# Performance work log

Hardware: AMD Instinct MI355X
Metric: run time of the kernel (lower is better)

Reference implementation:

```python
import jax, jax.numpy as jnp
import numpy as np


def _gcn(h, W, b, src, dst):
    # PyG GCNConv: x @ W, then symmetric-normalized aggregation over edges
    # (edge list already includes self-loops), bias added after.
    n = h.shape[0]
    deg = jnp.zeros((n,), h.dtype).at[dst].add(jnp.ones((), h.dtype))
    dinv = jnp.where(deg > 0, jax.lax.rsqrt(deg), jnp.zeros((), h.dtype))
    norm = dinv[src] * dinv[dst]  # [E]
    m = h @ W                     # [N, d_h]
    out = jnp.zeros_like(m).at[dst].add(norm[:, None] * m[src])
    return out + b


def setup_inputs() -> dict:
    key = jax.random.key(0)
    F, K = 1000, 100              # files, blocks per file
    N = F * K                     # total blocks
    D_SEM, D_STR = 768, 256
    D_H, D_SH, D_PR, NPROJ = 512, 256, 256, 100

    # sliding-window (window=2) edges within each file, bidirectional, + self loops
    base = np.arange(N)
    pos = base % K
    s_l, d_l = [], []
    for d in (1, 2):
        i = base[pos < K - d]
        j = i + d
        s_l += [i, j]
        d_l += [j, i]
    s_l.append(base)  # self loops (GCNConv add_self_loops)
    d_l.append(base)
    src = jnp.asarray(np.concatenate(s_l), dtype=jnp.int32)
    dst = jnp.asarray(np.concatenate(d_l), dtype=jnp.int32)
    seg_ids = jnp.asarray(base // K, dtype=jnp.int32)  # file id per block (CSR blk_ptr equivalent)

    ks = jax.random.split(key, 16)
    def w(k, shape):
        return jax.random.normal(k, shape, jnp.float32) * 0.02
    z = lambda n: jnp.zeros((n,), jnp.float32)

    return dict(
        h_sem=jax.random.normal(ks[0], (N, D_SEM), jnp.float32),
        e_struct=jax.random.normal(ks[1], (N, D_STR), jnp.float32),
        W_fusion=w(ks[2], (D_SEM + D_STR, D_H)), b_fusion=z(D_H),
        W_g1=w(ks[3], (D_H, D_H)), b_g1=z(D_H),
        W_g2=w(ks[4], (D_H, D_H)), b_g2=z(D_H),
        W_att=w(ks[5], (D_H, D_H)), b_att=z(D_H),
        context=w(ks[6], (D_H,)),
        W_sh1=w(ks[7], (D_H, D_SH)), b_sh1=z(D_SH),
        W_sh2=w(ks[8], (D_SH, D_SH)), b_sh2=z(D_SH),
        W_pr1=w(ks[9], (D_H, D_PR)), b_pr1=z(D_PR),
        W_pr2=w(ks[10], (D_PR, D_PR)), b_pr2=z(D_PR),
        W_dpr=w(ks[11], (D_PR, NPROJ)), b_dpr=z(NPROJ),
        W_bug=w(ks[12], (D_H, 1)), b_bug=z(1),
        src=src, dst=dst, seg_ids=seg_ids, num_files=F,
    )


def reference(h_sem, e_struct, W_fusion, b_fusion, W_g1, b_g1, W_g2, b_g2,
              W_att, b_att, context, W_sh1, b_sh1, W_sh2, b_sh2,
              W_pr1, b_pr1, W_pr2, b_pr2, W_dpr, b_dpr, W_bug, b_bug,
              src, dst, seg_ids, num_files):
    # fusion of semantic + structural features
    h0 = jnp.concatenate([h_sem, e_struct], axis=1) @ W_fusion + b_fusion  # [N, d_h]
    h1 = jax.nn.relu(_gcn(h0, W_g1, b_g1, src, dst))
    h_blk = _gcn(h1, W_g2, b_g2, src, dst)                                # [N, d_h]

    # ragged attention pooling over per-file segments (vectorized segment softmax)
    scores = jnp.tanh(h_blk @ W_att + b_att) @ context                    # [N]
    seg_max = jax.ops.segment_max(scores, seg_ids, num_segments=num_files)
    ex = jnp.exp(scores - seg_max[seg_ids])
    seg_sum = jax.ops.segment_sum(ex, seg_ids, num_segments=num_files)
    alpha = ex / seg_sum[seg_ids]                                         # [N]
    h_file = jax.ops.segment_sum(alpha[:, None] * h_blk, seg_ids,
                                 num_segments=num_files)                  # [F, d_h]

    z_sh = jax.nn.relu(h_file @ W_sh1 + b_sh1) @ W_sh2 + b_sh2            # [F, d_sh]
    z_pr = jax.nn.relu(h_file @ W_pr1 + b_pr1) @ W_pr2 + b_pr2            # [F, d_pr]
    logits_pr_dom = z_pr @ W_dpr + b_dpr                                  # [F, num_projects]
    logit_bug = h_file @ W_bug + b_bug                                    # [F, 1]
    loss_ortho = jnp.mean((z_sh.T @ z_pr) ** 2)                           # disentanglement penalty
    return (h_blk, alpha, h_file, z_sh, z_pr, logits_pr_dom, logit_bug, loss_ortho)
```

## Files before the change

### kernel.cpp

```cpp
#include <hip/hip_runtime.h>

typedef unsigned short u16;
typedef unsigned int   u32;
typedef __attribute__((ext_vector_type(8))) short  short8;
typedef __attribute__((ext_vector_type(4))) float  floatx4;

#define DEV __device__ __forceinline__

DEV float bf2f(u16 u){ return __uint_as_float(((u32)u) << 16); }
DEV u16 f2bf(float x){
  u32 u = __float_as_uint(x);
  u += 0x7FFFu + ((u >> 16) & 1u);
  return (u16)(u >> 16);
}
DEV float blo(u32 u){ return __uint_as_float(u << 16); }
DEV float bhi(u32 u){ return __uint_as_float(u & 0xffff0000u); }

DEV void async16(const void* g, void* l){
  __builtin_amdgcn_global_load_lds((__attribute__((address_space(1))) void*)g,
                                   (__attribute__((address_space(3))) void*)l,
                                   16, 0, 0);
}

constexpr int NN   = 100000;
constexpr int FF   = 1000;
constexpr int KPF  = 100;
constexpr int DH   = 512;

constexpr size_t OUT_HBLK  = 0;
constexpr size_t OUT_ALPHA = 51200000;
constexpr size_t OUT_HFILE = 51300000;
constexpr size_t OUT_ZSH   = 51812000;
constexpr size_t OUT_ZPR   = 52068000;
constexpr size_t OUT_LOG   = 52324000;
constexpr size_t OUT_BUG   = 52424000;
constexpr size_t OUT_LOSS  = 52425000;

constexpr size_t WS_A      = 0;
constexpr size_t WS_M1     = 0;
constexpr size_t WS_H1     = 102400000;
constexpr size_t WS_HBLK   = 0;
constexpr size_t WS_H0     = 204800000;
constexpr size_t WS_M2     = 204800000;
constexpr size_t WS_SCOREP = 307200000;
constexpr size_t WS_WT     = 308800000;
constexpr size_t WS_HFILEB = 312300000;
constexpr size_t WS_TSH    = 313400000;
constexpr size_t WS_TPR    = 314000000;
constexpr size_t WS_ZPRB   = 314600000;
constexpr size_t WS_ORTHOP = 315200000;

constexpr int WT_FUS = 0;
constexpr int WT_G1  = 524288;
constexpr int WT_G2  = 786432;
constexpr int WT_ATT = 1048576;
constexpr int WT_SH1 = 1310720;
constexpr int WT_SH2 = 1441792;
constexpr int WT_PR1 = 1507328;
constexpr int WT_PR2 = 1638400;
constexpr int WT_DPR = 1703936;
constexpr int WT_TOT = 1729536;

struct PrepTab {
  const float* src[9];
  int K[9];
  int N[9];
  int prefix[10];
};

__global__ __launch_bounds__(256) void prep_w(PrepTab t, u16* __restrict__ dst){
  int gid = blockIdx.x * 256 + threadIdx.x;
  if (gid >= t.prefix[9]) return;
  int i = 0;
  while (gid >= t.prefix[i+1]) ++i;
  int e  = gid - t.prefix[i];
  int Ni = t.N[i];
  int k  = e / Ni;
  int n  = e - k * Ni;
  dst[t.prefix[i] + (size_t)n * t.K[i] + k] = f2bf(t.src[i][(size_t)k * Ni + n]);
}

__global__ __launch_bounds__(256) void build_A(const float* __restrict__ hsem,
                                               const float* __restrict__ est,
                                               u16* __restrict__ out){
  int gid = blockIdx.x * 256 + threadIdx.x;
  int row = gid >> 7;
  int c   = (gid & 127) << 3;
  const float* src = (c < 768) ? (hsem + (size_t)row * 768 + c)
                               : (est  + (size_t)row * 256 + (c - 768));
  float4 v0 = *(const float4*)src;
  float4 v1 = *(const float4*)(src + 4);
  uint4 o;
  o.x = (u32)f2bf(v0.x) | ((u32)f2bf(v0.y) << 16);
  o.y = (u32)f2bf(v0.z) | ((u32)f2bf(v0.w) << 16);
  o.z = (u32)f2bf(v1.x) | ((u32)f2bf(v1.y) << 16);
  o.w = (u32)f2bf(v1.z) | ((u32)f2bf(v1.w) << 16);
  *(uint4*)(out + (size_t)row * 1024 + c) = o;
}

template<int MODE, bool BIAS>
__global__ __launch_bounds__(512, 2) void gemm256(
    const u16* __restrict__ A, const u16* __restrict__ B,
    int M, int N, int K,
    const float* __restrict__ bias,
    u16* __restrict__ outb,
    const float* __restrict__ ctx, float* __restrict__ scorep)
{
  extern __shared__ u16 S[];
  const int tid  = threadIdx.x;
  const int wid  = tid >> 6, lane = tid & 63;
  const int lq   = lane >> 4, lr = lane & 15;

  const int ny  = N >> 8;
  const int nwg = (int)gridDim.x;
  const int q   = nwg >> 3, r = nwg & 7;
  const int xcd = (int)blockIdx.x & 7, pos = (int)blockIdx.x >> 3;
  const int lid = (xcd < r ? xcd * (q + 1) : r * (q + 1) + (xcd - r) * q) + pos;
  const int ty  = lid % ny, tx = lid / ny;
  const int m0  = tx << 8, n0 = ty << 8;

  const int wr = wid >> 2, wc = wid & 3;
  const int wrow = wr << 7, wcol = wc << 6;

  const int srow = (wid << 3) + (lane >> 3);
  const int scol = ((lane & 7) ^ (lane >> 3)) << 3;
  const u16* pa[4];
  const u16* pb[4];
  #pragma unroll
  for (int h = 0; h < 2; ++h)
    #pragma unroll
    for (int j = 0; j < 2; ++j) {
      int ra = m0 + h * 128 + j * 64 + srow;  ra = min(ra, M - 1);
      int rb = n0 + h * 128 + j * 64 + srow;
      pa[h * 2 + j] = A + (size_t)ra * K + scol;
      pb[h * 2 + j] = B + (size_t)rb * K + scol;
    }

  auto STAGE = [&](int p){
    char* base = (char*)S + (p << 16) + (wid << 10);
    #pragma unroll
    for (int h = 0; h < 2; ++h)
      #pragma unroll
      for (int j = 0; j < 2; ++j) {
        async16(pa[h * 2 + j], base + h * 16384 + j * 8192);
        async16(pb[h * 2 + j], base + 32768 + h * 16384 + j * 8192);
        pa[h * 2 + j] += 64;  pb[h * 2 + j] += 64;
      }
  };

  floatx4 acc[8][4];
  #pragma unroll
  for (int i = 0; i < 8; ++i)
    #pragma unroll
    for (int j = 0; j < 4; ++j)
      acc[i][j] = floatx4{0.f, 0.f, 0.f, 0.f};

  const int NT = K >> 6;
  STAGE(0);
  STAGE(1);

  const int rsl = lr & 7;
  for (int kt = 0; kt < NT; ++kt) {
    if (kt + 1 < NT) asm volatile("s_waitcnt vmcnt(8)" ::: "memory");
    else             asm volatile("s_waitcnt vmcnt(0)" ::: "memory");
    __builtin_amdgcn_s_barrier();
    __builtin_amdgcn_sched_barrier(0);
    const u16* ap = S + ((kt & 1) << 15);
    const u16* bp = ap + 16384;
    #pragma unroll
    for (int k2 = 0; k2 < 2; ++k2) {
      short8 af[8], bf[4];
      const int sl = ((k2 << 2) | lq) ^ rsl;
      #pragma unroll
      for (int mi = 0; mi < 8; ++mi)
        af[mi] = *(const short8*)(ap + ((wrow + mi * 16 + lr) << 6) + (sl << 3));
      #pragma unroll
      for (int ni = 0; ni < 4; ++ni)
        bf[ni] = *(const short8*)(bp + ((wcol + ni * 16 + lr) << 6) + (sl << 3));
      __builtin_amdgcn_s_setprio(1);
      #pragma unroll
      for (int mi = 0; mi < 8; ++mi)
        #pragma unroll
        for (int ni = 0; ni < 4; ++ni)
          acc[mi][ni] = __builtin_amdgcn_mfma_f32_16x16x32_bf16(af[mi], bf[ni], acc[mi][ni], 0, 0, 0);
      __builtin_amdgcn_s_setprio(0);
    }
    __builtin_amdgcn_s_barrier();
    __builtin_amdgcn_sched_barrier(0);
    if (kt + 2 < NT) STAGE(kt & 1);
  }

  if constexpr (MODE == 3) {
    #pragma unroll
    for (int mi = 0; mi < 8; ++mi) {
      #pragma unroll
      for (int r2 = 0; r2 < 4; ++r2) {
        float psum = 0.f;
        #pragma unroll
        for (int ni = 0; ni < 4; ++ni) {
          int gc = n0 + wcol + ni * 16 + lr;
          psum += tanhf(acc[mi][ni][r2] + bias[gc]) * ctx[gc];
        }
        psum += __shfl_xor(psum, 1); psum += __shfl_xor(psum, 2);
        psum += __shfl_xor(psum, 4); psum += __shfl_xor(psum, 8);
        int gr = m0 + wrow + mi * 16 + (lq << 2) + r2;
        if (lr == 0 && gr < M) scorep[(size_t)ty * M + gr] = psum;
      }
    }
  } else {
    #pragma unroll
    for (int mi = 0; mi < 8; ++mi) {
      int grb = m0 + wrow + mi * 16 + (lq << 2);
      #pragma unroll
      for (int ni = 0; ni < 4; ++ni) {
        int gc = n0 + wcol + ni * 16 + lr;
        float bv = BIAS ? bias[gc] : 0.f;
        #pragma unroll
        for (int r2 = 0; r2 < 4; ++r2) {
          int gr = grb + r2;
          if (gr < M) outb[(size_t)gr * N + gc] = f2bf(acc[mi][ni][r2] + bv);
        }
      }
    }
  }
}

template<int MODE, bool BIAS, bool RELU>
__global__ __launch_bounds__(256) void gemm_bt(
    const u16* __restrict__ A, const u16* __restrict__ B,
    int M, int N, int K, int ny,
    const float* __restrict__ bias,
    u16* __restrict__ outb, float* __restrict__ outf,
    int ldc, int nvalid,
    const float* __restrict__ ctx, float* __restrict__ scorep)
{
  __shared__ u16 As[3 * 4096];
  __shared__ u16 Bs[3 * 4096];
  const int tid  = threadIdx.x;
  const int wave = tid >> 6, lane = tid & 63;

  const int nwg = (int)gridDim.x;
  const int q   = nwg >> 3, r = nwg & 7;
  const int xcd = (int)blockIdx.x & 7, pos = (int)blockIdx.x >> 3;
  const int lid = (xcd < r ? xcd * (q + 1) : r * (q + 1) + (xcd - r) * q) + pos;
  const int ty  = lid % ny, tx = lid / ny;
  const int m0  = tx << 7, n0 = ty << 7;

  const int wm = (wave & 1) << 6, wn = (wave >> 1) << 6;
  const int lq = lane >> 4, lr = lane & 15;

  floatx4 acc[4][4];
  #pragma unroll
  for (int i = 0; i < 4; ++i)
    #pragma unroll
    for (int j = 0; j < 4; ++j)
      acc[i][j] = floatx4{0.f, 0.f, 0.f, 0.f};

  int arow = m0 + (wave << 4) + (lane >> 2);
  int ar0 = min(arow, M - 1);
  int ar1 = min(arow + 64, M - 1);
  int brow = n0 + (wave << 4) + (lane >> 2);
  int br0 = min(brow, N - 1);
  int br1 = min(brow + 64, N - 1);
  const int kc = (((lane & 3) ^ ((lane >> 3) & 3)) << 3);
  const u16* ga0 = A + (size_t)ar0 * K + kc;
  const u16* ga1 = A + (size_t)ar1 * K + kc;
  const u16* gb0 = B + (size_t)br0 * K + kc;
  const u16* gb1 = B + (size_t)br1 * K + kc;

  auto STAGE = [&](int buf){
    u16* as = As + (buf << 12);
    u16* bs = Bs + (buf << 12);
    async16(ga0, as + (wave << 9));
    async16(ga1, as + 2048 + (wave << 9));
    async16(gb0, bs + (wave << 9));
    async16(gb1, bs + 2048 + (wave << 9));
    ga0 += 32; ga1 += 32; gb0 += 32; gb1 += 32;
  };

  const int nIt = K >> 5;
  STAGE(0);
  if (nIt > 1) STAGE(1);
  const int rsw = (lr >> 1) & 3;
  int bt = 0;
  for (int it = 0; it < nIt; ++it) {
    if (it + 1 < nIt) asm volatile("s_waitcnt vmcnt(4) lgkmcnt(0)" ::: "memory");
    else              asm volatile("s_waitcnt vmcnt(0) lgkmcnt(0)" ::: "memory");
    __builtin_amdgcn_s_barrier();
    __builtin_amdgcn_sched_barrier(0);
    if (it + 2 < nIt) { int b2 = bt + 2; if (b2 >= 3) b2 -= 3; STAGE(b2); }
    const u16* as = As + (bt << 12);
    const u16* bs = Bs + (bt << 12);
    short8 af[4], bfr[4];
    #pragma unroll
    for (int mi = 0; mi < 4; ++mi)
      af[mi] = *(const short8*)(as + ((wm + mi * 16 + lr) << 5) + ((lq ^ rsw) << 3));
    #pragma unroll
    for (int ni = 0; ni < 4; ++ni)
      bfr[ni] = *(const short8*)(bs + ((wn + ni * 16 + lr) << 5) + ((lq ^ rsw) << 3));
    #pragma unroll
    for (int mi = 0; mi < 4; ++mi)
      #pragma unroll
      for (int ni = 0; ni < 4; ++ni)
        acc[mi][ni] = __builtin_amdgcn_mfma_f32_16x16x32_bf16(af[mi], bfr[ni], acc[mi][ni], 0, 0, 0);
    if (++bt == 3) bt = 0;
  }

  if constexpr (MODE == 3) {
    #pragma unroll
    for (int mi = 0; mi < 4; ++mi) {
      #pragma unroll
      for (int r2 = 0; r2 < 4; ++r2) {
        float p = 0.f;
        #pragma unroll
        for (int ni = 0; ni < 4; ++ni) {
          int gc = n0 + wn + ni * 16 + lr;
          p += tanhf(acc[mi][ni][r2] + bias[gc]) * ctx[gc];
        }
        p += __shfl_xor(p, 1); p += __shfl_xor(p, 2);
        p += __shfl_xor(p, 4); p += __shfl_xor(p, 8);
        int gr = m0 + wm + mi * 16 + lq * 4 + r2;
        if (lr == 0 && gr < M) scorep[(size_t)ty * M + gr] = p;
      }
    }
  } else {
    #pragma unroll
    for (int mi = 0; mi < 4; ++mi) {
      int grb = m0 + wm + mi * 16 + lq * 4;
      #pragma unroll
      for (int ni = 0; ni < 4; ++ni) {
        int gc = n0 + wn + ni * 16 + lr;
        if (gc >= nvalid) continue;
        float bv = BIAS ? bias[gc] : 0.f;
        #pragma unroll
        for (int r2 = 0; r2 < 4; ++r2) {
          int gr = grb + r2;
          if (gr >= M) continue;
          float v = acc[mi][ni][r2] + bv;
          if (RELU) v = fmaxf(v, 0.f);
          if (MODE == 0 || MODE == 2) outb[(size_t)gr * ldc + gc] = f2bf(v);
          if (MODE == 1 || MODE == 2) outf[(size_t)gr * ldc + gc] = v;
        }
      }
    }
  }
}

DEV float dinv_of(int p){
  return rsqrtf((float)(1 + min(p, 2) + min(99 - p, 2)));
}

template<bool RELU, bool DUAL>
__global__ __launch_bounds__(256) void agg_k(const u16* __restrict__ m,
                                             const float* __restrict__ bias,
                                             u16* __restrict__ outb,
                                             float* __restrict__ outf){
  int gid = blockIdx.x * 256 + threadIdx.x;
  int row = gid >> 6;
  int c   = (gid & 63) << 3;
  int pos = row % KPF;
  float ds = dinv_of(pos);
  float a0=0,a1=0,a2=0,a3=0,a4=0,a5=0,a6=0,a7=0;
  #pragma unroll
  for (int d = -2; d <= 2; ++d) {
    int p2 = pos + d;
    if (p2 < 0 || p2 >= KPF) continue;
    float w = ds * dinv_of(p2);
    uint4 v = *(const uint4*)(m + (size_t)(row + d) * DH + c);
    a0 += w * blo(v.x); a1 += w * bhi(v.x);
    a2 += w * blo(v.y); a3 += w * bhi(v.y);
    a4 += w * blo(v.z); a5 += w * bhi(v.z);
    a6 += w * blo(v.w); a7 += w * bhi(v.w);
  }
  float o[8] = {a0,a1,a2,a3,a4,a5,a6,a7};
  #pragma unroll
  for (int j = 0; j < 8; ++j) {
    o[j] += bias[c + j];
    if (RELU) o[j] = fmaxf(o[j], 0.f);
  }
  uint4 st;
  st.x = (u32)f2bf(o[0]) | ((u32)f2bf(o[1]) << 16);
  st.y = (u32)f2bf(o[2]) | ((u32)f2bf(o[3]) << 16);
  st.z = (u32)f2bf(o[4]) | ((u32)f2bf(o[5]) << 16);
  st.w = (u32)f2bf(o[6]) | ((u32)f2bf(o[7]) << 16);
  *(uint4*)(outb + (size_t)row * DH + c) = st;
  if (DUAL) {
    float4 f0 = {o[0], o[1], o[2], o[3]};
    float4 f1 = {o[4], o[5], o[6], o[7]};
    *(float4*)(outf + (size_t)row * DH + c)     = f0;
    *(float4*)(outf + (size_t)row * DH + c + 4) = f1;
  }
}

__global__ __launch_bounds__(256) void pool_k(const float* __restrict__ sp,
                                              const u16* __restrict__ hblk,
                                              float* __restrict__ alpha_out,
                                              float* __restrict__ hfile_f,
                                              u16* __restrict__ hfile_b){
  int f = blockIdx.x, tid = threadIdx.x;
  __shared__ float sAl[KPF];
  __shared__ float red[8];
  float s = -INFINITY;
  if (tid < KPF) {
    int r = f * KPF + tid;
    s = sp[r] + sp[NN + r];
  }
  float mx = s;
  for (int off = 32; off >= 1; off >>= 1) mx = fmaxf(mx, __shfl_xor(mx, off));
  if ((tid & 63) == 0) red[tid >> 6] = mx;
  __syncthreads();
  mx = fmaxf(fmaxf(red[0], red[1]), fmaxf(red[2], red[3]));
  float ex = (tid < KPF) ? expf(s - mx) : 0.f;
  float sm = ex;
  for (int off = 32; off >= 1; off >>= 1) sm += __shfl_xor(sm, off);
  if ((tid & 63) == 0) red[4 + (tid >> 6)] = sm;
  __syncthreads();
  sm = red[4] + red[5] + red[6] + red[7];
  float al = ex / sm;
  if (tid < KPF) { alpha_out[(size_t)f * KPF + tid] = al; sAl[tid] = al; }
  __syncthreads();
  const u16* base = hblk + (size_t)f * KPF * DH;
  float acc0 = 0.f, acc1 = 0.f;
  for (int i = 0; i < KPF; ++i) {
    float w = sAl[i];
    acc0 += w * bf2f(base[i * DH + tid]);
    acc1 += w * bf2f(base[i * DH + 256 + tid]);
  }
  hfile_f[(size_t)f * DH + tid]       = acc0;
  hfile_f[(size_t)f * DH + 256 + tid] = acc1;
  hfile_b[(size_t)f * DH + tid]       = f2bf(acc0);
  hfile_b[(size_t)f * DH + 256 + tid] = f2bf(acc1);
}

__global__ __launch_bounds__(256) void bug_k(const float* __restrict__ hfile,
                                             const float* __restrict__ w,
                                             const float* __restrict__ b,
                                             float* __restrict__ out){
  int row  = blockIdx.x * 4 + (threadIdx.x >> 6);
  int lane = threadIdx.x & 63;
  const float* h = hfile + (size_t)row * DH;
  float s = 0.f;
  #pragma unroll
  for (int j = 0; j < 8; ++j) s += h[lane + j * 64] * w[lane + j * 64];
  for (int off = 32; off >= 1; off >>= 1) s += __shfl_xor(s, off);
  if (lane == 0) out[row] = s + b[0];
}

__global__ __launch_bounds__(256) void ortho_k(const float* __restrict__ zsh,
                                               const float* __restrict__ zpr,
                                               float* __restrict__ part){
  int bi = blockIdx.x >> 4, bj = blockIdx.x & 15;
  int ty = threadIdx.x >> 4, tx = threadIdx.x & 15;
  __shared__ float sa[64 * 16], sb[64 * 16];
  float acc = 0.f;
  for (int k0 = 0; k0 < FF; k0 += 64) {
    #pragma unroll
    for (int q = 0; q < 4; ++q) {
      int kk = ty + q * 16;
      int k  = k0 + kk;
      float va = 0.f, vb = 0.f;
      if (k < FF) {
        va = zsh[(size_t)k * 256 + bi * 16 + tx];
        vb = zpr[(size_t)k * 256 + bj * 16 + tx];
      }
      sa[kk * 16 + tx] = va;
      sb[kk * 16 + tx] = vb;
    }
    __syncthreads();
    #pragma unroll 8
    for (int kk = 0; kk < 64; ++kk) acc += sa[kk * 16 + ty] * sb[kk * 16 + tx];
    __syncthreads();
  }
  float ssq = acc * acc;
  for (int off = 32; off >= 1; off >>= 1) ssq += __shfl_xor(ssq, off);
  __shared__ float r[4];
  if ((threadIdx.x & 63) == 0) r[threadIdx.x >> 6] = ssq;
  __syncthreads();
  if (threadIdx.x == 0) part[blockIdx.x] = r[0] + r[1] + r[2] + r[3];
}

__global__ __launch_bounds__(256) void ortho_fin(const float* __restrict__ part,
                                                 float* __restrict__ out){
  int tid = threadIdx.x;
  float s = part[tid];
  for (int off = 32; off >= 1; off >>= 1) s += __shfl_xor(s, off);
  __shared__ float r[4];
  if ((tid & 63) == 0) r[tid >> 6] = s;
  __syncthreads();
  if (tid == 0) out[0] = (r[0] + r[1] + r[2] + r[3]) * (1.0f / 65536.0f);
}

extern "C" void kernel_launch(void* const* d_in, const int* in_sizes, int n_in,
                              void* d_out, int out_size, void* d_ws, size_t ws_size,
                              hipStream_t stream) {
  const float* h_sem    = (const float*)d_in[0];
  const float* e_struct = (const float*)d_in[1];
  const float* W_fusion = (const float*)d_in[2];
  const float* b_fusion = (const float*)d_in[3];
  const float* W_g1     = (const float*)d_in[4];
  const float* b_g1     = (const float*)d_in[5];
  const float* W_g2     = (const float*)d_in[6];
  const float* b_g2     = (const float*)d_in[7];
  const float* W_att    = (const float*)d_in[8];
  const float* b_att    = (const float*)d_in[9];
  const float* context  = (const float*)d_in[10];
  const float* W_sh1    = (const float*)d_in[11];
  const float* b_sh1    = (const float*)d_in[12];
  const float* W_sh2    = (const float*)d_in[13];
  const float* b_sh2    = (const float*)d_in[14];
  const float* W_pr1    = (const float*)d_in[15];
  const float* b_pr1    = (const float*)d_in[16];
  const float* W_pr2    = (const float*)d_in[17];
  const float* b_pr2    = (const float*)d_in[18];
  const float* W_dpr    = (const float*)d_in[19];
  const float* b_dpr    = (const float*)d_in[20];
  const float* W_bug    = (const float*)d_in[21];
  const float* b_bug    = (const float*)d_in[22];

  char*  ws  = (char*)d_ws;
  float* out = (float*)d_out;

  u16*   Abf    = (u16*)(ws + WS_A);
  u16*   h0b    = (u16*)(ws + WS_H0);
  u16*   m1b    = (u16*)(ws + WS_M1);
  u16*   h1b    = (u16*)(ws + WS_H1);
  u16*   m2b    = (u16*)(ws + WS_M2);
  u16*   hblkb  = (u16*)(ws + WS_HBLK);
  float* scorep = (float*)(ws + WS_SCOREP);
  u16*   WT     = (u16*)(ws + WS_WT);
  u16*   hfileb = (u16*)(ws + WS_HFILEB);
  u16*   tshb   = (u16*)(ws + WS_TSH);
  u16*   tprb   = (u16*)(ws + WS_TPR);
  u16*   zprb   = (u16*)(ws + WS_ZPRB);
  float* opart  = (float*)(ws + WS_ORTHOP);

  PrepTab t;
  const float* srcs[9] = {W_fusion, W_g1, W_g2, W_att, W_sh1, W_sh2, W_pr1, W_pr2, W_dpr};
  int Ks[9] = {1024, 512, 512, 512, 512, 256, 512, 256, 256};
  int Ns[9] = {512, 512, 512, 512, 256, 256, 256, 256, 100};
  int pre[10] = {WT_FUS, WT_G1, WT_G2, WT_ATT, WT_SH1, WT_SH2, WT_PR1, WT_PR2, WT_DPR, WT_TOT};
  for (int i = 0; i < 9; ++i) { t.src[i] = srcs[i]; t.K[i] = Ks[i]; t.N[i] = Ns[i]; }
  for (int i = 0; i < 10; ++i) t.prefix[i] = pre[i];
  prep_w<<<(WT_TOT + 255) / 256, 256, 0, stream>>>(t, WT);

  build_A<<<NN * 128 / 256, 256, 0, stream>>>(h_sem, e_struct, Abf);

  gemm256<0, true><<<391 * 2, 512, 131072, stream>>>(
      Abf, WT + WT_FUS, NN, 512, 1024, b_fusion, h0b, nullptr, nullptr);

  gemm256<0, false><<<391 * 2, 512, 131072, stream>>>(
      h0b, WT + WT_G1, NN, 512, 512, nullptr, m1b, nullptr, nullptr);

  agg_k<true, false><<<NN * 64 / 256, 256, 0, stream>>>(m1b, b_g1, h1b, nullptr);

  gemm256<0, false><<<391 * 2, 512, 131072, stream>>>(
      h1b, WT + WT_G2, NN, 512, 512, nullptr, m2b, nullptr, nullptr);

  agg_k<false, true><<<NN * 64 / 256, 256, 0, stream>>>(m2b, b_g2, hblkb, out + OUT_HBLK);

  gemm256<3, true><<<391 * 2, 512, 131072, stream>>>(
      hblkb, WT + WT_ATT, NN, 512, 512, b_att, nullptr, context, scorep);

  pool_k<<<FF, 256, 0, stream>>>(scorep, hblkb, out + OUT_ALPHA, out + OUT_HFILE, hfileb);

  gemm_bt<0, true, true><<<8 * 2, 256, 0, stream>>>(
      hfileb, WT + WT_SH1, FF, 256, 512, 2, b_sh1, tshb, nullptr, 256, 256, nullptr, nullptr);
  gemm_bt<1, true, false><<<8 * 2, 256, 0, stream>>>(
      tshb, WT + WT_SH2, FF, 256, 256, 2, b_sh2, nullptr, out + OUT_ZSH, 256, 256, nullptr, nullptr);
  gemm_bt<0, true, true><<<8 * 2, 256, 0, stream>>>(
      hfileb, WT + WT_PR1, FF, 256, 512, 2, b_pr1, tprb, nullptr, 256, 256, nullptr, nullptr);
  gemm_bt<2, true, false><<<8 * 2, 256, 0, stream>>>(
      tprb, WT + WT_PR2, FF, 256, 256, 2, b_pr2, zprb, out + OUT_ZPR, 256, 256, nullptr, nullptr);
  gemm_bt<1, true, false><<<8 * 1, 256, 0, stream>>>(
      zprb, WT + WT_DPR, FF, 100, 256, 1, b_dpr, nullptr, out + OUT_LOG, 100, 100, nullptr, nullptr);

  bug_k<<<FF / 4, 256, 0, stream>>>(out + OUT_HFILE, W_bug, b_bug, out + OUT_BUG);

  ortho_k<<<256, 256, 0, stream>>>(out + OUT_ZSH, out + OUT_ZPR, opart);
  ortho_fin<<<1, 256, 0, stream>>>(opart, out + OUT_LOSS);
}
```

Before: 1.462 ms.

## Halve gemm256 K-tile to cut LDS and raise occupancy; vectorize epilogues

The main 256x256 GEMM now stages 32-wide K slices instead of 64, using 64KB of static LDS in place of 128KB of dynamic LDS. Launch bounds go from 2 to 4 workgroups per CU to raise occupancy. MFMA operands are swapped so each lane holds four consecutive columns, which lets the epilogue write packed 8-byte bf16 stores and load bias as float4. The attention-score epilogue now reduces across the four column waves through an LDS buffer and a __syncthreads instead of storing per-wave partials. The cost is twice as many barriers and K iterations per tile, and the 128 accumulator registers per lane may spill under the tighter register budget.

```diff
diff --git a/kernel.cpp b/kernel.cpp
--- a/kernel.cpp
+++ b/kernel.cpp
@@ -99,14 +99,15 @@
 }
 
 template<int MODE, bool BIAS>
-__global__ __launch_bounds__(512, 2) void gemm256(
+__global__ __launch_bounds__(512, 4) void gemm256(
     const u16* __restrict__ A, const u16* __restrict__ B,
     int M, int N, int K,
     const float* __restrict__ bias,
     u16* __restrict__ outb,
     const float* __restrict__ ctx, float* __restrict__ scorep)
 {
-  extern __shared__ u16 S[];
+  __shared__ u16 S[2 * 16384];
+  __shared__ float red[8 * 128];
   const int tid  = threadIdx.x;
   const int wid  = tid >> 6, lane = tid & 63;
   const int lq   = lane >> 4, lr = lane & 15;
@@ -122,30 +123,22 @@
   const int wr = wid >> 2, wc = wid & 3;
   const int wrow = wr << 7, wcol = wc << 6;
 
-  const int srow = (wid << 3) + (lane >> 3);
-  const int scol = ((lane & 7) ^ (lane >> 3)) << 3;
-  const u16* pa[4];
-  const u16* pb[4];
-  #pragma unroll
-  for (int h = 0; h < 2; ++h)
-    #pragma unroll
-    for (int j = 0; j < 2; ++j) {
-      int ra = m0 + h * 128 + j * 64 + srow;  ra = min(ra, M - 1);
-      int rb = n0 + h * 128 + j * 64 + srow;
-      pa[h * 2 + j] = A + (size_t)ra * K + scol;
-      pb[h * 2 + j] = B + (size_t)rb * K + scol;
-    }
+  const int g = (((lane & 3) ^ ((lane >> 3) & 3)) << 3);
+  int ra0 = m0 + (wid << 5) + (lane >> 2);
+  int ra1 = min(ra0 + 16, M - 1);
+  ra0 = min(ra0, M - 1);
+  const int rb0 = n0 + (wid << 5) + (lane >> 2);
+  const u16* pa0 = A + (size_t)ra0 * K + g;
+  const u16* pa1 = A + (size_t)ra1 * K + g;
+  const u16* pb0 = B + (size_t)rb0 * K + g;
+  const u16* pb1 = B + (size_t)(rb0 + 16) * K + g;
 
   auto STAGE = [&](int p){
-    char* base = (char*)S + (p << 16) + (wid << 10);
-    #pragma unroll
-    for (int h = 0; h < 2; ++h)
-      #pragma unroll
-      for (int j = 0; j < 2; ++j) {
-        async16(pa[h * 2 + j], base + h * 16384 + j * 8192);
-        async16(pb[h * 2 + j], base + 32768 + h * 16384 + j * 8192);
-        pa[h * 2 + j] += 64;  pb[h * 2 + j] += 64;
-      }
+    u16* ab = S + (p << 14) + (wid << 10);
+    u16* bb = ab + 8192;
+    async16(pa0, ab); async16(pa1, ab + 512);
+    async16(pb0, bb); async16(pb1, bb + 512);
+    pa0 += 32; pa1 += 32; pb0 += 32; pb1 += 32;
   };
 
   floatx4 acc[8][4];
@@ -155,71 +148,93 @@
     for (int j = 0; j < 4; ++j)
       acc[i][j] = floatx4{0.f, 0.f, 0.f, 0.f};
 
-  const int NT = K >> 6;
+  const int NT = K >> 5;
   STAGE(0);
   STAGE(1);
 
-  const int rsl = lr & 7;
+  const int rs = (lr >> 1) & 3;
   for (int kt = 0; kt < NT; ++kt) {
-    if (kt + 1 < NT) asm volatile("s_waitcnt vmcnt(8)" ::: "memory");
+    if (kt + 1 < NT) asm volatile("s_waitcnt vmcnt(4)" ::: "memory");
     else             asm volatile("s_waitcnt vmcnt(0)" ::: "memory");
     __builtin_amdgcn_s_barrier();
     __builtin_amdgcn_sched_barrier(0);
-    const u16* ap = S + ((kt & 1) << 15);
-    const u16* bp = ap + 16384;
-    #pragma unroll
-    for (int k2 = 0; k2 < 2; ++k2) {
-      short8 af[8], bf[4];
-      const int sl = ((k2 << 2) | lq) ^ rsl;
-      #pragma unroll
-      for (int mi = 0; mi < 8; ++mi)
-        af[mi] = *(const short8*)(ap + ((wrow + mi * 16 + lr) << 6) + (sl << 3));
+    const u16* ap = S + ((kt & 1) << 14);
+    const u16* bp = ap + 8192;
+    short8 af[8], bf[4];
+    const int sl = (lq ^ rs) << 3;
+    #pragma unroll
+    for (int mi = 0; mi < 8; ++mi)
+      af[mi] = *(const short8*)(ap + ((wrow + mi * 16 + lr) << 5) + sl);
+    #pragma unroll
+    for (int ni = 0; ni < 4; ++ni)
+      bf[ni] = *(const short8*)(bp + ((wcol + ni * 16 + lr) << 5) + sl);
+    __builtin_amdgcn_s_setprio(1);
+    #pragma unroll
+    for (int mi = 0; mi < 8; ++mi)
       #pragma unroll
       for (int ni = 0; ni < 4; ++ni)
-        bf[ni] = *(const short8*)(bp + ((wcol + ni * 16 + lr) << 6) + (sl << 3));
-      __builtin_amdgcn_s_setprio(1);
-      #pragma unroll
-      for (int mi = 0; mi < 8; ++mi)
-        #pragma unroll
-        for (int ni = 0; ni < 4; ++ni)
-          acc[mi][ni] = __builtin_amdgcn_mfma_f32_16x16x32_bf16(af[mi], bf[ni], acc[mi][ni], 0, 0, 0);
-      __builtin_amdgcn_s_setprio(0);
-    }
+        acc[mi][ni] = __builtin_amdgcn_mfma_f32_16x16x32_bf16(bf[ni], af[mi], acc[mi][ni], 0, 0, 0);
+    __builtin_amdgcn_s_setprio(0);
     __builtin_amdgcn_s_barrier();
     __builtin_amdgcn_sched_barrier(0);
     if (kt + 2 < NT) STAGE(kt & 1);
   }
 
   if constexpr (MODE == 3) {
+    float bvv[16], cvv[16];
+    #pragma unroll
+    for (int ni = 0; ni < 4; ++ni) {
+      int gc0 = n0 + wcol + ni * 16 + (lq << 2);
+      float4 b4 = *(const float4*)(bias + gc0);
+      float4 c4 = *(const float4*)(ctx + gc0);
+      bvv[ni*4+0] = b4.x; bvv[ni*4+1] = b4.y; bvv[ni*4+2] = b4.z; bvv[ni*4+3] = b4.w;
+      cvv[ni*4+0] = c4.x; cvv[ni*4+1] = c4.y; cvv[ni*4+2] = c4.z; cvv[ni*4+3] = c4.w;
+    }
     #pragma unroll
     for (int mi = 0; mi < 8; ++mi) {
-      #pragma unroll
-      for (int r2 = 0; r2 < 4; ++r2) {
-        float psum = 0.f;
+      float p = 0.f;
+      #pragma unroll
+      for (int ni = 0; ni < 4; ++ni)
         #pragma unroll
-        for (int ni = 0; ni < 4; ++ni) {
-          int gc = n0 + wcol + ni * 16 + lr;
-          psum += tanhf(acc[mi][ni][r2] + bias[gc]) * ctx[gc];
-        }
-        psum += __shfl_xor(psum, 1); psum += __shfl_xor(psum, 2);
-        psum += __shfl_xor(psum, 4); psum += __shfl_xor(psum, 8);
-        int gr = m0 + wrow + mi * 16 + (lq << 2) + r2;
-        if (lr == 0 && gr < M) scorep[(size_t)ty * M + gr] = psum;
+        for (int r2 = 0; r2 < 4; ++r2)
+          p += tanhf(acc[mi][ni][r2] + bvv[ni*4+r2]) * cvv[ni*4+r2];
+      p += __shfl_xor(p, 16);
+      p += __shfl_xor(p, 32);
+      if (lq == 0) red[wid * 128 + mi * 16 + lr] = p;
+    }
+    __syncthreads();
+    if (wc == 0) {
+      #pragma unroll
+      for (int h = 0; h < 2; ++h) {
+        int rr = lane + h * 64;
+        int base = (wr << 2) * 128 + rr;
+        float s4 = red[base] + red[base + 128] + red[base + 256] + red[base + 384];
+        int gr = m0 + (wr << 7) + rr;
+        if (gr < M) scorep[(size_t)ty * M + gr] = s4;
       }
     }
   } else {
+    float4 bv[4];
+    #pragma unroll
+    for (int ni = 0; ni < 4; ++ni) {
+      if (BIAS) bv[ni] = *(const float4*)(bias + n0 + wcol + ni * 16 + (lq << 2));
+      else      bv[ni] = make_float4(0.f, 0.f, 0.f, 0.f);
+    }
     #pragma unroll
     for (int mi = 0; mi < 8; ++mi) {
-      int grb = m0 + wrow + mi * 16 + (lq << 2);
+      int gr = m0 + wrow + mi * 16 + lr;
+      if (gr >= M) continue;
+      u16* rp = outb + (size_t)gr * N;
       #pragma unroll
       for (int ni = 0; ni < 4; ++ni) {
-        int gc = n0 + wcol + ni * 16 + lr;
-        float bv = BIAS ? bias[gc] : 0.f;
-        #pragma unroll
-        for (int r2 = 0; r2 < 4; ++r2) {
-          int gr = grb + r2;
-          if (gr < M) outb[(size_t)gr * N + gc] = f2bf(acc[mi][ni][r2] + bv);
-        }
+        float v0 = acc[mi][ni][0] + bv[ni].x;
+        float v1 = acc[mi][ni][1] + bv[ni].y;
+        float v2 = acc[mi][ni][2] + bv[ni].z;
+        float v3 = acc[mi][ni][3] + bv[ni].w;
+        uint2 st;
+        st.x = (u32)f2bf(v0) | ((u32)f2bf(v1) << 16);
+        st.y = (u32)f2bf(v2) | ((u32)f2bf(v3) << 16);
+        *(uint2*)(rp + n0 + wcol + ni * 16 + (lq << 2)) = st;
       }
     }
   }
@@ -545,20 +560,20 @@
 
   build_A<<<NN * 128 / 256, 256, 0, stream>>>(h_sem, e_struct, Abf);
 
-  gemm256<0, true><<<391 * 2, 512, 131072, stream>>>(
+  gemm256<0, true><<<391 * 2, 512, 0, stream>>>(
       Abf, WT + WT_FUS, NN, 512, 1024, b_fusion, h0b, nullptr, nullptr);
 
-  gemm256<0, false><<<391 * 2, 512, 131072, stream>>>(
+  gemm256<0, false><<<391 * 2, 512, 0, stream>>>(
       h0b, WT + WT_G1, NN, 512, 512, nullptr, m1b, nullptr, nullptr);
 
   agg_k<true, false><<<NN * 64 / 256, 256, 0, stream>>>(m1b, b_g1, h1b, nullptr);
 
-  gemm256<0, false><<<391 * 2, 512, 131072, stream>>>(
+  gemm256<0, false><<<391 * 2, 512, 0, stream>>>(
       h1b, WT + WT_G2, NN, 512, 512, nullptr, m2b, nullptr, nullptr);
 
   agg_k<false, true><<<NN * 64 / 256, 256, 0, stream>>>(m2b, b_g2, hblkb, out + OUT_HBLK);
 
-  gemm256<3, true><<<391 * 2, 512, 131072, stream>>>(
+  gemm256<3, true><<<391 * 2, 512, 0, stream>>>(
       hblkb, WT + WT_ATT, NN, 512, 512, b_att, nullptr, context, scorep);
 
   pool_k<<<FF, 256, 0, stream>>>(scorep, hblkb, out + OUT_ALPHA, out + OUT_HFILE, hfileb);
```

Result: slower. 4.333 ms (+196.3%).
